# Kernel tuning notes

Measured on AMD Instinct MI355X. Metric: run time of the kernel, lower is better.

The kernel has to match this reference:

```python
import jax, jax.numpy as jnp
import numpy as np

REGION1 = REGION2 = 64
OVERLAP1 = OVERLAP2 = 0
MAX_M1 = MAX_M2 = 16


def dht1(x, axis):
    # 1D discrete Hartley transform along `axis` (real - imag of FFT)
    X = jnp.fft.fft(x, axis=axis)
    return X.real - X.imag


def dht2(x):
    # 2D DHT over last two axes
    X = jnp.fft.fft2(x, axes=(-2, -1))
    return X.real - X.imag


def flip_periodic2(x):
    # Faithful to torch code: flatten last two dims jointly, keep element 0, flip the rest
    s = x.shape
    n = s[-2] * s[-1]
    xf = x.reshape(s[:-2] + (n,))
    zf = jnp.concatenate([xf[..., :1], xf[..., 1:][..., ::-1]], axis=-1)
    return zf.reshape(s)


def hartley_conv2(x, y):
    # x: [b, i, h, w], y: [i, o, h, w] -> [b, o, h, w]; conv via Hartley theorem then idht
    X = dht2(x)
    Y = dht2(y)
    Xf = flip_periodic2(X)
    Yf = flip_periodic2(Y)
    Ye = 0.5 * (Y + Yf)
    Yo = 0.5 * (Y - Yf)
    Z = jnp.einsum('bihw,iohw->bohw', X, Ye) + jnp.einsum('bihw,iohw->bohw', Xf, Yo)
    n = x.shape[-2] * x.shape[-1]
    return dht2(Z) / n  # idht2 (DHT is involutory up to 1/n)


def spectral_conv2d(x, error_np, weights):
    B, Cin, S1, S2 = x.shape
    Cout = weights.shape[1]
    stride1 = REGION1 - OVERLAP1
    stride2 = REGION2 - OVERLAP2
    nr1 = (S1 - OVERLAP1) // stride1 + (1 if (S1 - OVERLAP1) % stride1 else 0)
    nr2 = (S2 - OVERLAP2) // stride2 + (1 if (S2 - OVERLAP2) % stride2 else 0)
    out = jnp.zeros((B, Cout, S1, S2), x.dtype)
    counts = np.zeros((S1, S2), np.float32)
    for i in range(nr1):
        for j in range(nr2):
            s1 = i * stride1; e1 = s1 + REGION1
            if e1 > S1:
                e1 = S1; s1 = max(e1 - REGION1, 0)
            s2 = j * stride2; e2 = s2 + REGION2
            if e2 > S2:
                e2 = S2; s2 = max(e2 - REGION2, 0)
            region_x = x[:, :, s1:e1, s2:e2]
            # adaptive per-sample mode counts from error signal (static, numpy)
            avg = error_np[:, s1:e1, s2:e2].mean(axis=(1, 2))
            mn, mx = avg.min(), avg.max()
            norm = (avg - mn) / (mx - mn) if (mx - mn) > 1e-8 else np.zeros_like(avg)
            nm1 = np.minimum((norm * (MAX_M1 - 1)).astype(np.int64) + 1, MAX_M1)
            nm2 = np.minimum((norm * (MAX_M2 - 1)).astype(np.int64) + 1, MAX_M2)
            # separable per-axis DHT of the region
            region_ht = dht1(dht1(region_x, -2), -1)
            out_ht = jnp.zeros((B, Cout, REGION1, REGION2), x.dtype)
            for b in range(B):
                n1 = int(nm1[b]); n2 = int(nm2[b])
                blk = hartley_conv2(region_ht[b:b + 1, :, :n1, :n2], weights[:, :, :n1, :n2])
                out_ht = out_ht.at[b, :, :n1, :n2].set(blk[0])
            # separable inverse per-axis DHT: dht1 along each axis / region area
            region_out = dht1(dht1(out_ht, -2), -1) / (REGION1 * REGION2)
            out = out.at[:, :, s1:e1, s2:e2].add(region_out)
            counts[s1:e1, s2:e2] += 1
    counts[counts == 0] = 1
    return out / jnp.asarray(counts, x.dtype)


def setup_inputs() -> dict:
    key = jax.random.key(0)
    k1, k2, k3 = jax.random.split(key, 3)
    B, Cin, Cout, S = 8, 32, 32, 256
    scale = 1.0 / (Cin * Cout)
    x = jax.random.normal(k1, (B, Cin, S, S), dtype=jnp.float32)
    error_signal = jax.random.uniform(k2, (B, S, S), dtype=jnp.float32)
    weights = scale * jax.random.uniform(k3, (Cin, Cout, MAX_M1, MAX_M2), dtype=jnp.float32)
    return {"x": x, "error_signal": error_signal, "weights": weights}


def reference(x, error_signal, weights):
    error_np = np.asarray(error_signal)
    return spectral_conv2d(x, error_np, weights)
```

## Files before the change

kernel.cpp:

```cpp
#include <hip/hip_runtime.h>
#include <math.h>

#define NB 8
#define CIN 32
#define COUT 32
#define SS 256
#define REG 64
#define NMAX 16

#define AVG_OFF   0
#define C64_OFF   4096
#define CN_OFF    4352
#define Y_OFF     8192
#define YF_OFF    (8u << 20)
#define XE_OFF    (16u << 20)
#define XO_OFF    (20u << 20)

__device__ __constant__ int CPS16[17] =
    {0, 0, 4, 8, 20, 36, 64, 100, 152, 216, 300, 400, 524, 668, 840, 1036, 1264};

__device__ __forceinline__ int region_n(const float* __restrict__ avg, int r, int b) {
    float mn = avg[r * 8], mx = mn;
    for (int bb = 1; bb < NB; ++bb) {
        float v = avg[r * 8 + bb];
        mn = fminf(mn, v);
        mx = fmaxf(mx, v);
    }
    float d = mx - mn;
    bool ok = ((double)d > 1e-8);
    float norm = ok ? (avg[r * 8 + b] - mn) / d : 0.0f;
    float tt = norm * 15.0f;
    int nv = (int)tt + 1;
    return nv > NMAX ? NMAX : nv;
}

__global__ void k_prep(const float* __restrict__ err, const float* __restrict__ wts,
                       float* __restrict__ avg, float* __restrict__ cyc64,
                       float* __restrict__ cycN, float* __restrict__ Y,
                       float* __restrict__ Yf) {
    int bx = blockIdx.x;
    int t = threadIdx.x;

    if (bx < 128) {
        int r = bx & 15, b = bx >> 4;
        int ri = r >> 2, rj = r & 3;
        const float* base = err + ((size_t)b * SS + ri * REG) * SS + rj * REG;
        double s = 0.0;
        for (int it = 0; it < 4; ++it) {
            int f = it * 256 + t;
            int u = f >> 4, c4 = f & 15;
            float4 v = *(const float4*)(base + (size_t)u * SS + c4 * 4);
            s += (double)v.x + (double)v.y + (double)v.z + (double)v.w;
        }
        __shared__ double sm[256];
        sm[t] = s;
        __syncthreads();
        for (int w = 128; w > 0; w >>= 1) {
            if (t < w) sm[t] += sm[t + w];
            __syncthreads();
        }
        if (t == 0) avg[r * 8 + b] = (float)(sm[0] / 4096.0);
        return;
    }

    if (bx == 128) {
        if (t < 64) {
            double a = (2.0 * M_PI / 64.0) * (double)t;
            cyc64[t] = (float)(cos(a) + sin(a));
        } else if (t < 64 + 136) {
            int e = t - 64;
            int n = 1;
            while (n * (n + 1) / 2 <= e) ++n;
            int j = e - n * (n - 1) / 2;
            double a = (2.0 * M_PI / (double)n) * (double)j;
            cycN[e] = (float)(cos(a) + sin(a));
        }
        return;
    }

    int io = bx - 129;
    __shared__ float Wt[256];
    __shared__ float T1[256];
    __shared__ float T2[256];
    __shared__ float cnAll[136];
    if (t < 136) {
        int e = t;
        int n = 1;
        while (n * (n + 1) / 2 <= e) ++n;
        int j = e - n * (n - 1) / 2;
        double a = (2.0 * M_PI / (double)n) * (double)j;
        cnAll[e] = (float)(cos(a) + sin(a));
    }
    Wt[t] = wts[(size_t)io * 256 + t];
    __syncthreads();

    for (int n = 1; n <= NMAX; ++n) {
        int nn = n * n;
        int nnp = (nn + 3) & ~3;
        const float* cnL = &cnAll[(n * (n - 1)) / 2];
        int p = 0, q = 0;
        if (t < nn) { p = t / n; q = t - p * n; }
        if (t < nn) {
            float acc = 0.f;
            int idx = 0;
            for (int v = 0; v < n; ++v) {
                acc += Wt[p * 16 + v] * cnL[idx];
                idx += q; if (idx >= n) idx -= n;
            }
            T1[p * n + q] = acc;
        }
        __syncthreads();
        if (t < nn) {
            float acc = 0.f;
            int idx = 0;
            for (int u = 0; u < n; ++u) {
                acc += T1[u * n + q] * cnL[idx];
                idx += p; if (idx >= n) idx -= n;
            }
            T2[t] = acc;
        }
        __syncthreads();
        size_t basei = (size_t)1024 * CPS16[n] + (size_t)io * nnp;
        if (t < nn) {
            int pf = (p == 0) ? 0 : n - p;
            int qf = (q == 0) ? 0 : n - q;
            float v = 0.5f * (T2[p * n + q] + T2[pf * n + q] + T2[p * n + qf] - T2[pf * n + qf]);
            Y[basei + t] = v;
            int fk = (t == 0) ? 0 : nn - t;
            Yf[basei + fk] = v;
        } else if (t < nnp) {
            Y[basei + t]  = 0.f;
            Yf[basei + t] = 0.f;
        }
        __syncthreads();
    }
}

__global__ void k_fwd(const float* __restrict__ x, const float* __restrict__ avg,
                      const float* __restrict__ cyc64, const float* __restrict__ cycN,
                      float* __restrict__ Xe, float* __restrict__ Xo) {
    int i = blockIdx.x, r = blockIdx.y, b = blockIdx.z;
    int n = region_n(avg, r, b);
    int nn = n * n;
    int ri = r >> 2, rj = r & 3;
    int t = threadIdx.x;

    __shared__ __align__(16) float R[64 * 64];
    __shared__ __align__(16) float M1[16 * 68];
    __shared__ float H[256];
    __shared__ float T1[256];
    __shared__ float T2[256];
    __shared__ float cyc64L[64];
    __shared__ float cnL[16];

    if (t < 64) cyc64L[t] = cyc64[t];
    if (t < n)  cnL[t] = cycN[(n * (n - 1)) / 2 + t];

    const float* base = x + (((size_t)(b * CIN + i)) * SS + ri * REG) * SS + rj * REG;
    float4* R4 = (float4*)R;
    {
        int u0 = t >> 4, c4 = t & 15;
        for (int it = 0; it < 4; ++it) {
            int u = it * 16 + u0;
            R4[u * 16 + c4] = *(const float4*)(base + (size_t)u * SS + c4 * 4);
        }
    }
    __syncthreads();

    {
        int uq = t >> 6, ps = (t >> 4) & 3, vg = t & 15;
        int p0 = ps, p1 = ps + 4, p2 = ps + 8, p3 = ps + 12;
        int i0 = (p0 * (uq << 4)) & 63;
        int i1 = (p1 * (uq << 4)) & 63;
        int i2 = (p2 * (uq << 4)) & 63;
        int i3 = (p3 * (uq << 4)) & 63;
        float4 a0 = {0.f,0.f,0.f,0.f}, a1 = a0, a2 = a0, a3 = a0;
        int ubase = (uq << 4) * 16 + vg;
        for (int uu = 0; uu < 16; ++uu) {
            float4 rv = R4[ubase + uu * 16];
            if (p0 < n) { float c = cyc64L[i0];
                a0.x += c*rv.x; a0.y += c*rv.y; a0.z += c*rv.z; a0.w += c*rv.w; }
            if (p1 < n) { float c = cyc64L[i1];
                a1.x += c*rv.x; a1.y += c*rv.y; a1.z += c*rv.z; a1.w += c*rv.w; }
            if (p2 < n) { float c = cyc64L[i2];
                a2.x += c*rv.x; a2.y += c*rv.y; a2.z += c*rv.z; a2.w += c*rv.w; }
            if (p3 < n) { float c = cyc64L[i3];
                a3.x += c*rv.x; a3.y += c*rv.y; a3.z += c*rv.z; a3.w += c*rv.w; }
            i0 = (i0 + p0) & 63; i1 = (i1 + p1) & 63;
            i2 = (i2 + p2) & 63; i3 = (i3 + p3) & 63;
        }
        __syncthreads();
        float4* P4 = R4;
        int pb = (uq << 8) + vg;
        if (p0 < n) P4[pb + p0 * 16] = a0;
        if (p1 < n) P4[pb + p1 * 16] = a1;
        if (p2 < n) P4[pb + p2 * 16] = a2;
        if (p3 < n) P4[pb + p3 * 16] = a3;
        __syncthreads();
        int pr = t >> 4, vr = t & 15;
        if (pr < n) {
            float4 q0 = P4[pr * 16 + vr];
            float4 q1 = P4[256 + pr * 16 + vr];
            float4 q2 = P4[512 + pr * 16 + vr];
            float4 q3 = P4[768 + pr * 16 + vr];
            float4 s;
            s.x = (q0.x + q1.x) + (q2.x + q3.x);
            s.y = (q0.y + q1.y) + (q2.y + q3.y);
            s.z = (q0.z + q1.z) + (q2.z + q3.z);
            s.w = (q0.w + q1.w) + (q2.w + q3.w);
            *(float4*)&M1[pr * 68 + vr * 4] = s;
        }
    }
    __syncthreads();

    int p = 0, q = 0;
    if (t < nn) { p = t / n; q = t - p * n; }

    if (t < nn) {
        float acc = 0.f;
        int idx = 0;
        for (int v = 0; v < 64; ++v) {
            acc += M1[p * 68 + v] * cyc64L[idx];
            idx = (idx + q) & 63;
        }
        H[t] = acc;
    }
    __syncthreads();

    if (t < nn) {
        float acc = 0.f;
        int idx = 0;
        for (int v = 0; v < n; ++v) {
            acc += H[p * n + v] * cnL[idx];
            idx += q; if (idx >= n) idx -= n;
        }
        T1[p * n + q] = acc;
    }
    __syncthreads();
    if (t < nn) {
        float acc = 0.f;
        int idx = 0;
        for (int u = 0; u < n; ++u) {
            acc += T1[u * n + q] * cnL[idx];
            idx += p; if (idx >= n) idx -= n;
        }
        T2[t] = acc;
    }
    __syncthreads();
    if (t < nn) {
        int pf = (p == 0) ? 0 : n - p;
        int qf = (q == 0) ? 0 : n - q;
        H[t] = 0.5f * (T2[p * n + q] + T2[pf * n + q] + T2[p * n + qf] - T2[pf * n + qf]);
    }
    __syncthreads();

    {
        size_t o = (((size_t)(b * 16 + r)) * CIN + i) * 256 + t;
        if (t < nn) {
            int fk = (t == 0) ? 0 : nn - t;
            float a = H[t], c = H[fk];
            Xe[o] = 0.5f * (a + c);
            Xo[o] = 0.5f * (a - c);
        } else {
            Xe[o] = 0.f;
            Xo[o] = 0.f;
        }
    }
}

__global__ void k_zout(const float* __restrict__ Xe, const float* __restrict__ Xo,
                       const float* __restrict__ Y, const float* __restrict__ Yf,
                       const float* __restrict__ avg, const float* __restrict__ cyc64,
                       const float* __restrict__ cycN, float* __restrict__ out) {
    int o  = blockIdx.x;
    int br = blockIdx.y;
    int b = br >> 4, r = br & 15;
    int n = region_n(avg, r, b);
    int nn = n * n;
    int nnp4 = (nn + 3) >> 2;
    int t = threadIdx.x;

    __shared__ __align__(16) float zpart[4][256];
    __shared__ float Zs[256];
    __shared__ float T1[256];
    __shared__ float T2[256];
    __shared__ float Bk[256];
    __shared__ __align__(16) float E1[16 * 64];
    __shared__ __align__(16) float CTo[16 * 16 * 4];
    __shared__ float cyc64L[64];
    __shared__ float cnL[16];

    if (t < 64) cyc64L[t] = cyc64[t];
    if (t < n)  cnL[t] = cycN[(n * (n - 1)) / 2 + t];

    int ig = t >> 6, s = t & 63;
    if (s < nnp4) {
        const float4* Yb4  = (const float4*)(Y  + (size_t)1024 * CPS16[n]);
        const float4* Yfb4 = (const float4*)(Yf + (size_t)1024 * CPS16[n]);
        const float4* Xe4 = (const float4*)(Xe + (size_t)br * CIN * 256);
        const float4* Xo4 = (const float4*)(Xo + (size_t)br * CIN * 256);
        float4 a = {0.f, 0.f, 0.f, 0.f};
#pragma unroll 4
        for (int ii = 0; ii < 8; ++ii) {
            int i = ig * 8 + ii;
            float4 xe = Xe4[i * 64 + s];
            float4 xo = Xo4[i * 64 + s];
            int yo = (i * COUT + o) * nnp4 + s;
            float4 y  = Yb4[yo];
            float4 yf = Yfb4[yo];
            a.x += xe.x * y.x + xo.x * yf.x;
            a.y += xe.y * y.y + xo.y * yf.y;
            a.z += xe.z * y.z + xo.z * yf.z;
            a.w += xe.w * y.w + xo.w * yf.w;
        }
        *(float4*)&zpart[ig][4 * s] = a;
    }
    __syncthreads();

    {
        int pp = t >> 4, u0 = t & 15;
        float4 c;
        c.x = cyc64L[(pp * u0) & 63];
        c.y = cyc64L[(pp * (u0 + 16)) & 63];
        c.z = cyc64L[(pp * (u0 + 32)) & 63];
        c.w = cyc64L[(pp * (u0 + 48)) & 63];
        *(float4*)&CTo[t * 4] = c;
    }
    if (t < nn)
        Zs[t] = (zpart[0][t] + zpart[1][t]) + (zpart[2][t] + zpart[3][t]);

    int p = 0, q = 0;
    if (t < nn) { p = t / n; q = t - p * n; }
    __syncthreads();

    if (t < nn) {
        float acc = 0.f;
        int idx = 0;
        for (int v = 0; v < n; ++v) {
            acc += Zs[p * n + v] * cnL[idx];
            idx += q; if (idx >= n) idx -= n;
        }
        T1[p * n + q] = acc;
    }
    __syncthreads();
    if (t < nn) {
        float acc = 0.f;
        int idx = 0;
        for (int u = 0; u < n; ++u) {
            acc += T1[u * n + q] * cnL[idx];
            idx += p; if (idx >= n) idx -= n;
        }
        T2[t] = acc;
    }
    __syncthreads();
    if (t < nn) {
        int pf = (p == 0) ? 0 : n - p;
        int qf = (q == 0) ? 0 : n - q;
        Bk[t] = 0.5f * (T2[p * n + q] + T2[pf * n + q] + T2[p * n + qf] - T2[pf * n + qf])
                / (float)nn;
    }
    __syncthreads();

    for (int mm = t; mm < n * 64; mm += 256) {
        int pp = mm >> 6, v = mm & 63;
        float acc = 0.f;
        int idx = 0;
        for (int qq = 0; qq < n; ++qq) {
            acc += Bk[pp * n + qq] * cyc64L[idx];
            idx = (idx + v) & 63;
        }
        E1[pp * 64 + v] = acc;
    }
    __syncthreads();

    int ri = r >> 2, rj = r & 3;
    float* ob = out + (((size_t)(b * COUT + o)) * SS + ri * REG) * SS + rj * REG;
    const float4* E14 = (const float4*)E1;
    const float4* CT4 = (const float4*)CTo;
    const float inv = 1.0f / 4096.0f;
    int u0 = t >> 4, vg = t & 15;
    float4 aA = {0.f,0.f,0.f,0.f}, aB = aA, aC = aA, aD = aA;
    for (int pp = 0; pp < n; ++pp) {
        float4 e = E14[pp * 16 + vg];
        float4 c = CT4[pp * 16 + u0];
        aA.x += c.x*e.x; aA.y += c.x*e.y; aA.z += c.x*e.z; aA.w += c.x*e.w;
        aB.x += c.y*e.x; aB.y += c.y*e.y; aB.z += c.y*e.z; aB.w += c.y*e.w;
        aC.x += c.z*e.x; aC.y += c.z*e.y; aC.z += c.z*e.z; aC.w += c.z*e.w;
        aD.x += c.w*e.x; aD.y += c.w*e.y; aD.z += c.w*e.z; aD.w += c.w*e.w;
    }
    aA.x *= inv; aA.y *= inv; aA.z *= inv; aA.w *= inv;
    aB.x *= inv; aB.y *= inv; aB.z *= inv; aB.w *= inv;
    aC.x *= inv; aC.y *= inv; aC.z *= inv; aC.w *= inv;
    aD.x *= inv; aD.y *= inv; aD.z *= inv; aD.w *= inv;
    *(float4*)(ob + (size_t)(u0)      * SS + vg * 4) = aA;
    *(float4*)(ob + (size_t)(16 + u0) * SS + vg * 4) = aB;
    *(float4*)(ob + (size_t)(32 + u0) * SS + vg * 4) = aC;
    *(float4*)(ob + (size_t)(48 + u0) * SS + vg * 4) = aD;
}

extern "C" void kernel_launch(void* const* d_in, const int* in_sizes, int n_in,
                              void* d_out, int out_size, void* d_ws, size_t ws_size,
                              hipStream_t stream) {
    const float* x   = (const float*)d_in[0];
    const float* err = (const float*)d_in[1];
    const float* wts = (const float*)d_in[2];
    float* out = (float*)d_out;
    char* ws = (char*)d_ws;

    float* avg   = (float*)(ws + AVG_OFF);
    float* cyc64 = (float*)(ws + C64_OFF);
    float* cycN  = (float*)(ws + CN_OFF);
    float* Y     = (float*)(ws + Y_OFF);
    float* Yf    = (float*)(ws + YF_OFF);
    float* Xe    = (float*)(ws + XE_OFF);
    float* Xo    = (float*)(ws + XO_OFF);

    k_prep<<<dim3(128 + 1 + CIN * COUT), 256, 0, stream>>>(err, wts, avg, cyc64, cycN, Y, Yf);
    k_fwd<<<dim3(CIN, 16, NB), 256, 0, stream>>>(x, avg, cyc64, cycN, Xe, Xo);
    k_zout<<<dim3(COUT, 128), 256, 0, stream>>>(Xe, Xo, Y, Yf, avg, cyc64, cycN, out);
}
```

Measured before the change: 179.2 us.

## Move weight DHT into forward kernel, add n==1 fast path, trim padded writes

Weight Hartley-transform work (1024 blocks) moves out of the prep kernel and into extra blocks of the forward kernel, reusing the region shared buffer. The weight work then runs alongside the input transforms instead of serialising before them, and the prep kernel keeps only the error averages and twiddle tables. The forward kernel now writes only the padded nn entries of Xe/Xo instead of all 256, and k_zout gets a constant-fill shortcut when a region uses one mode. Risk: zout may read stale Xe entries past nnp if it indexes beyond the padded count.

```diff
diff --git a/kernel.cpp b/kernel.cpp
--- a/kernel.cpp
+++ b/kernel.cpp
@@ -34,10 +34,8 @@
     return nv > NMAX ? NMAX : nv;
 }
 
-__global__ void k_prep(const float* __restrict__ err, const float* __restrict__ wts,
-                       float* __restrict__ avg, float* __restrict__ cyc64,
-                       float* __restrict__ cycN, float* __restrict__ Y,
-                       float* __restrict__ Yf) {
+__global__ void k_prep(const float* __restrict__ err, float* __restrict__ avg,
+                       float* __restrict__ cyc64, float* __restrict__ cycN) {
     int bx = blockIdx.x;
     int t = threadIdx.x;
 
@@ -63,86 +61,24 @@
         return;
     }
 
-    if (bx == 128) {
-        if (t < 64) {
-            double a = (2.0 * M_PI / 64.0) * (double)t;
-            cyc64[t] = (float)(cos(a) + sin(a));
-        } else if (t < 64 + 136) {
-            int e = t - 64;
-            int n = 1;
-            while (n * (n + 1) / 2 <= e) ++n;
-            int j = e - n * (n - 1) / 2;
-            double a = (2.0 * M_PI / (double)n) * (double)j;
-            cycN[e] = (float)(cos(a) + sin(a));
-        }
-        return;
-    }
-
-    int io = bx - 129;
-    __shared__ float Wt[256];
-    __shared__ float T1[256];
-    __shared__ float T2[256];
-    __shared__ float cnAll[136];
-    if (t < 136) {
-        int e = t;
+    if (t < 64) {
+        double a = (2.0 * M_PI / 64.0) * (double)t;
+        cyc64[t] = (float)(cos(a) + sin(a));
+    } else if (t < 64 + 136) {
+        int e = t - 64;
         int n = 1;
         while (n * (n + 1) / 2 <= e) ++n;
         int j = e - n * (n - 1) / 2;
         double a = (2.0 * M_PI / (double)n) * (double)j;
-        cnAll[e] = (float)(cos(a) + sin(a));
-    }
-    Wt[t] = wts[(size_t)io * 256 + t];
-    __syncthreads();
-
-    for (int n = 1; n <= NMAX; ++n) {
-        int nn = n * n;
-        int nnp = (nn + 3) & ~3;
-        const float* cnL = &cnAll[(n * (n - 1)) / 2];
-        int p = 0, q = 0;
-        if (t < nn) { p = t / n; q = t - p * n; }
-        if (t < nn) {
-            float acc = 0.f;
-            int idx = 0;
-            for (int v = 0; v < n; ++v) {
-                acc += Wt[p * 16 + v] * cnL[idx];
-                idx += q; if (idx >= n) idx -= n;
-            }
-            T1[p * n + q] = acc;
-        }
-        __syncthreads();
-        if (t < nn) {
-            float acc = 0.f;
-            int idx = 0;
-            for (int u = 0; u < n; ++u) {
-                acc += T1[u * n + q] * cnL[idx];
-                idx += p; if (idx >= n) idx -= n;
-            }
-            T2[t] = acc;
-        }
-        __syncthreads();
-        size_t basei = (size_t)1024 * CPS16[n] + (size_t)io * nnp;
-        if (t < nn) {
-            int pf = (p == 0) ? 0 : n - p;
-            int qf = (q == 0) ? 0 : n - q;
-            float v = 0.5f * (T2[p * n + q] + T2[pf * n + q] + T2[p * n + qf] - T2[pf * n + qf]);
-            Y[basei + t] = v;
-            int fk = (t == 0) ? 0 : nn - t;
-            Yf[basei + fk] = v;
-        } else if (t < nnp) {
-            Y[basei + t]  = 0.f;
-            Yf[basei + t] = 0.f;
-        }
-        __syncthreads();
+        cycN[e] = (float)(cos(a) + sin(a));
     }
 }
 
-__global__ void k_fwd(const float* __restrict__ x, const float* __restrict__ avg,
-                      const float* __restrict__ cyc64, const float* __restrict__ cycN,
-                      float* __restrict__ Xe, float* __restrict__ Xo) {
-    int i = blockIdx.x, r = blockIdx.y, b = blockIdx.z;
-    int n = region_n(avg, r, b);
-    int nn = n * n;
-    int ri = r >> 2, rj = r & 3;
+__global__ void k_fwd(const float* __restrict__ x, const float* __restrict__ wts,
+                      const float* __restrict__ avg, const float* __restrict__ cyc64,
+                      const float* __restrict__ cycN, float* __restrict__ Xe,
+                      float* __restrict__ Xo, float* __restrict__ Y,
+                      float* __restrict__ Yf) {
     int t = threadIdx.x;
 
     __shared__ __align__(16) float R[64 * 64];
@@ -152,6 +88,72 @@
     __shared__ float T2[256];
     __shared__ float cyc64L[64];
     __shared__ float cnL[16];
+
+    if (blockIdx.x >= CIN) {
+        int io = ((blockIdx.x - CIN) * 16 + blockIdx.y) * 8 + blockIdx.z;
+        float* Wt    = R;
+        float* T1w   = R + 256;
+        float* T2w   = R + 512;
+        float* cnAll = R + 768;
+        if (t < 136) {
+            int e = t;
+            int n = 1;
+            while (n * (n + 1) / 2 <= e) ++n;
+            int j = e - n * (n - 1) / 2;
+            double a = (2.0 * M_PI / (double)n) * (double)j;
+            cnAll[e] = (float)(cos(a) + sin(a));
+        }
+        Wt[t] = wts[(size_t)io * 256 + t];
+        __syncthreads();
+
+        for (int n = 1; n <= NMAX; ++n) {
+            int nn = n * n;
+            int nnp = (nn + 3) & ~3;
+            const float* cn = &cnAll[(n * (n - 1)) / 2];
+            int p = 0, q = 0;
+            if (t < nn) { p = t / n; q = t - p * n; }
+            if (t < nn) {
+                float acc = 0.f;
+                int idx = 0;
+                for (int v = 0; v < n; ++v) {
+                    acc += Wt[p * 16 + v] * cn[idx];
+                    idx += q; if (idx >= n) idx -= n;
+                }
+                T1w[p * n + q] = acc;
+            }
+            __syncthreads();
+            if (t < nn) {
+                float acc = 0.f;
+                int idx = 0;
+                for (int u = 0; u < n; ++u) {
+                    acc += T1w[u * n + q] * cn[idx];
+                    idx += p; if (idx >= n) idx -= n;
+                }
+                T2w[t] = acc;
+            }
+            __syncthreads();
+            size_t basei = (size_t)1024 * CPS16[n] + (size_t)io * nnp;
+            if (t < nn) {
+                int pf = (p == 0) ? 0 : n - p;
+                int qf = (q == 0) ? 0 : n - q;
+                float v = 0.5f * (T2w[p * n + q] + T2w[pf * n + q] + T2w[p * n + qf] - T2w[pf * n + qf]);
+                Y[basei + t] = v;
+                int fk = (t == 0) ? 0 : nn - t;
+                Yf[basei + fk] = v;
+            } else if (t < nnp) {
+                Y[basei + t]  = 0.f;
+                Yf[basei + t] = 0.f;
+            }
+            __syncthreads();
+        }
+        return;
+    }
+
+    int i = blockIdx.x, r = blockIdx.y, b = blockIdx.z;
+    int n = region_n(avg, r, b);
+    int nn = n * n;
+    int nnp = (nn + 3) & ~3;
+    int ri = r >> 2, rj = r & 3;
 
     if (t < 64) cyc64L[t] = cyc64[t];
     if (t < n)  cnL[t] = cycN[(n * (n - 1)) / 2 + t];
@@ -254,7 +256,7 @@
     }
     __syncthreads();
 
-    {
+    if (t < nnp) {
         size_t o = (((size_t)(b * 16 + r)) * CIN + i) * 256 + t;
         if (t < nn) {
             int fk = (t == 0) ? 0 : nn - t;
@@ -317,13 +319,28 @@
     }
     __syncthreads();
 
+    int ri = r >> 2, rj = r & 3;
+    int u0 = t >> 4, vg = t & 15;
+
+    if (n == 1) {
+        float val = ((zpart[0][0] + zpart[1][0]) + (zpart[2][0] + zpart[3][0]))
+                    * (1.0f / 4096.0f);
+        float4 vv = {val, val, val, val};
+        float* ob = out + (((size_t)(b * COUT + o)) * SS + ri * REG) * SS + rj * REG;
+        *(float4*)(ob + (size_t)(u0)      * SS + vg * 4) = vv;
+        *(float4*)(ob + (size_t)(16 + u0) * SS + vg * 4) = vv;
+        *(float4*)(ob + (size_t)(32 + u0) * SS + vg * 4) = vv;
+        *(float4*)(ob + (size_t)(48 + u0) * SS + vg * 4) = vv;
+        return;
+    }
+
     {
-        int pp = t >> 4, u0 = t & 15;
+        int pp = t >> 4, ub = t & 15;
         float4 c;
-        c.x = cyc64L[(pp * u0) & 63];
-        c.y = cyc64L[(pp * (u0 + 16)) & 63];
-        c.z = cyc64L[(pp * (u0 + 32)) & 63];
-        c.w = cyc64L[(pp * (u0 + 48)) & 63];
+        c.x = cyc64L[(pp * ub) & 63];
+        c.y = cyc64L[(pp * (ub + 16)) & 63];
+        c.z = cyc64L[(pp * (ub + 32)) & 63];
+        c.w = cyc64L[(pp * (ub + 48)) & 63];
         *(float4*)&CTo[t * 4] = c;
     }
     if (t < nn)
@@ -373,12 +390,10 @@
     }
     __syncthreads();
 
-    int ri = r >> 2, rj = r & 3;
     float* ob = out + (((size_t)(b * COUT + o)) * SS + ri * REG) * SS + rj * REG;
     const float4* E14 = (const float4*)E1;
     const float4* CT4 = (const float4*)CTo;
     const float inv = 1.0f / 4096.0f;
-    int u0 = t >> 4, vg = t & 15;
     float4 aA = {0.f,0.f,0.f,0.f}, aB = aA, aC = aA, aD = aA;
     for (int pp = 0; pp < n; ++pp) {
         float4 e = E14[pp * 16 + vg];
@@ -415,7 +430,8 @@
     float* Xe    = (float*)(ws + XE_OFF);
     float* Xo    = (float*)(ws + XO_OFF);
 
-    k_prep<<<dim3(128 + 1 + CIN * COUT), 256, 0, stream>>>(err, wts, avg, cyc64, cycN, Y, Yf);
-    k_fwd<<<dim3(CIN, 16, NB), 256, 0, stream>>>(x, avg, cyc64, cycN, Xe, Xo);
+    k_prep<<<dim3(129), 256, 0, stream>>>(err, avg, cyc64, cycN);
+    k_fwd<<<dim3(CIN + 8, 16, NB), 256, 0, stream>>>(x, wts, avg, cyc64, cycN,
+                                                     Xe, Xo, Y, Yf);
     k_zout<<<dim3(COUT, 128), 256, 0, stream>>>(Xe, Xo, Y, Yf, avg, cyc64, cycN, out);
 }
```

Result: slower. 187.0 us (+4.4%).

## Stream region rows from global in forward DHT, skip zero writes, fast n==1 path

Applied to the files above, without the earlier changes.

The forward kernel no longer stages the 64x64 region tile in a 16KB shared buffer. Each thread now streams rows straight from global memory and accumulates only the n needed output rows, which removes the cross-thread reduction and two barriers. This cuts shared memory use so more blocks can be resident, at the cost of idle threads when n is small and no reuse of data across threads. Zero padding of Xe/Xo is now written only up to the padded n*n, and a shortcut in k_zout handles n==1 regions by writing a constant value without running the inverse transform.

```diff
diff --git a/kernel.cpp b/kernel.cpp
--- a/kernel.cpp
+++ b/kernel.cpp
@@ -142,10 +142,10 @@
     int i = blockIdx.x, r = blockIdx.y, b = blockIdx.z;
     int n = region_n(avg, r, b);
     int nn = n * n;
+    int nnp = (nn + 3) & ~3;
     int ri = r >> 2, rj = r & 3;
     int t = threadIdx.x;
 
-    __shared__ __align__(16) float R[64 * 64];
     __shared__ __align__(16) float M1[16 * 68];
     __shared__ float H[256];
     __shared__ float T1[256];
@@ -155,60 +155,23 @@
 
     if (t < 64) cyc64L[t] = cyc64[t];
     if (t < n)  cnL[t] = cycN[(n * (n - 1)) / 2 + t];
+    __syncthreads();
 
     const float* base = x + (((size_t)(b * CIN + i)) * SS + ri * REG) * SS + rj * REG;
-    float4* R4 = (float4*)R;
+
     {
-        int u0 = t >> 4, c4 = t & 15;
-        for (int it = 0; it < 4; ++it) {
-            int u = it * 16 + u0;
-            R4[u * 16 + c4] = *(const float4*)(base + (size_t)u * SS + c4 * 4);
-        }
-    }
-    __syncthreads();
-
-    {
-        int uq = t >> 6, ps = (t >> 4) & 3, vg = t & 15;
-        int p0 = ps, p1 = ps + 4, p2 = ps + 8, p3 = ps + 12;
-        int i0 = (p0 * (uq << 4)) & 63;
-        int i1 = (p1 * (uq << 4)) & 63;
-        int i2 = (p2 * (uq << 4)) & 63;
-        int i3 = (p3 * (uq << 4)) & 63;
-        float4 a0 = {0.f,0.f,0.f,0.f}, a1 = a0, a2 = a0, a3 = a0;
-        int ubase = (uq << 4) * 16 + vg;
-        for (int uu = 0; uu < 16; ++uu) {
-            float4 rv = R4[ubase + uu * 16];
-            if (p0 < n) { float c = cyc64L[i0];
-                a0.x += c*rv.x; a0.y += c*rv.y; a0.z += c*rv.z; a0.w += c*rv.w; }
-            if (p1 < n) { float c = cyc64L[i1];
-                a1.x += c*rv.x; a1.y += c*rv.y; a1.z += c*rv.z; a1.w += c*rv.w; }
-            if (p2 < n) { float c = cyc64L[i2];
-                a2.x += c*rv.x; a2.y += c*rv.y; a2.z += c*rv.z; a2.w += c*rv.w; }
-            if (p3 < n) { float c = cyc64L[i3];
-                a3.x += c*rv.x; a3.y += c*rv.y; a3.z += c*rv.z; a3.w += c*rv.w; }
-            i0 = (i0 + p0) & 63; i1 = (i1 + p1) & 63;
-            i2 = (i2 + p2) & 63; i3 = (i3 + p3) & 63;
-        }
-        __syncthreads();
-        float4* P4 = R4;
-        int pb = (uq << 8) + vg;
-        if (p0 < n) P4[pb + p0 * 16] = a0;
-        if (p1 < n) P4[pb + p1 * 16] = a1;
-        if (p2 < n) P4[pb + p2 * 16] = a2;
-        if (p3 < n) P4[pb + p3 * 16] = a3;
-        __syncthreads();
-        int pr = t >> 4, vr = t & 15;
-        if (pr < n) {
-            float4 q0 = P4[pr * 16 + vr];
-            float4 q1 = P4[256 + pr * 16 + vr];
-            float4 q2 = P4[512 + pr * 16 + vr];
-            float4 q3 = P4[768 + pr * 16 + vr];
-            float4 s;
-            s.x = (q0.x + q1.x) + (q2.x + q3.x);
-            s.y = (q0.y + q1.y) + (q2.y + q3.y);
-            s.z = (q0.z + q1.z) + (q2.z + q3.z);
-            s.w = (q0.w + q1.w) + (q2.w + q3.w);
-            *(float4*)&M1[pr * 68 + vr * 4] = s;
+        int p1 = t >> 4, vg = t & 15;
+        if (p1 < n) {
+            float4 acc = {0.f, 0.f, 0.f, 0.f};
+            int idx = 0;
+            const float* cb = base + vg * 4;
+            for (int u = 0; u < 64; ++u) {
+                float c = cyc64L[idx]; idx = (idx + p1) & 63;
+                float4 rv = *(const float4*)(cb + (size_t)u * SS);
+                acc.x += c * rv.x; acc.y += c * rv.y;
+                acc.z += c * rv.z; acc.w += c * rv.w;
+            }
+            *(float4*)&M1[p1 * 68 + vg * 4] = acc;
         }
     }
     __syncthreads();
@@ -254,7 +217,7 @@
     }
     __syncthreads();
 
-    {
+    if (t < nnp) {
         size_t o = (((size_t)(b * 16 + r)) * CIN + i) * 256 + t;
         if (t < nn) {
             int fk = (t == 0) ? 0 : nn - t;
@@ -317,13 +280,28 @@
     }
     __syncthreads();
 
+    int ri = r >> 2, rj = r & 3;
+    int u0 = t >> 4, vg = t & 15;
+
+    if (n == 1) {
+        float val = ((zpart[0][0] + zpart[1][0]) + (zpart[2][0] + zpart[3][0]))
+                    * (1.0f / 4096.0f);
+        float4 vv = {val, val, val, val};
+        float* ob = out + (((size_t)(b * COUT + o)) * SS + ri * REG) * SS + rj * REG;
+        *(float4*)(ob + (size_t)(u0)      * SS + vg * 4) = vv;
+        *(float4*)(ob + (size_t)(16 + u0) * SS + vg * 4) = vv;
+        *(float4*)(ob + (size_t)(32 + u0) * SS + vg * 4) = vv;
+        *(float4*)(ob + (size_t)(48 + u0) * SS + vg * 4) = vv;
+        return;
+    }
+
     {
-        int pp = t >> 4, u0 = t & 15;
+        int pp = t >> 4, ub = t & 15;
         float4 c;
-        c.x = cyc64L[(pp * u0) & 63];
-        c.y = cyc64L[(pp * (u0 + 16)) & 63];
-        c.z = cyc64L[(pp * (u0 + 32)) & 63];
-        c.w = cyc64L[(pp * (u0 + 48)) & 63];
+        c.x = cyc64L[(pp * ub) & 63];
+        c.y = cyc64L[(pp * (ub + 16)) & 63];
+        c.z = cyc64L[(pp * (ub + 32)) & 63];
+        c.w = cyc64L[(pp * (ub + 48)) & 63];
         *(float4*)&CTo[t * 4] = c;
     }
     if (t < nn)
@@ -373,12 +351,10 @@
     }
     __syncthreads();
 
-    int ri = r >> 2, rj = r & 3;
     float* ob = out + (((size_t)(b * COUT + o)) * SS + ri * REG) * SS + rj * REG;
     const float4* E14 = (const float4*)E1;
     const float4* CT4 = (const float4*)CTo;
     const float inv = 1.0f / 4096.0f;
-    int u0 = t >> 4, vg = t & 15;
     float4 aA = {0.f,0.f,0.f,0.f}, aB = aA, aC = aA, aD = aA;
     for (int pp = 0; pp < n; ++pp) {
         float4 e = E14[pp * 16 + vg];
```

Result: slower. 208.2 us (+16.2%).
